# Optimization experiments

Measured on AMD Instinct MI355X. Metric: run time of the kernel, lower is better.

The kernel has to match this reference:

```python
import jax, jax.numpy as jnp
import numpy as np

ALPHA = 0.2  # LeakyReLU negative slope
NEG = -1e10  # mask value, matches -10000000000.0


def _gat_head(feat, adj, W, a1, a2):
    # feat: [N, Fin], W: [Fin, Fout], a1/a2: [Fout]
    h = feat @ W                              # [N, Fout]
    s = h @ a1                                # [N] attn_for_self
    t = h @ a2                                # [N] attn_for_neighs
    logits = jax.nn.leaky_relu(s[:, None] + t[None, :], ALPHA)  # [N, N]
    logits = logits + NEG * (1.0 - adj)       # additive adjacency mask
    attn = jax.nn.softmax(logits, axis=-1)    # [N, N]
    return attn @ h                           # [N, Fout]


def setup_inputs() -> dict:
    key = jax.random.key(0)
    ks = jax.random.split(key, 9)
    N, NFEAT, NHID, NCLASS, H = 6144, 128, 64, 16, 4
    glorot = jax.nn.initializers.glorot_uniform()
    adj = (jax.random.uniform(ks[0], (N, N)) < 0.005).astype(jnp.float32)
    feature = jax.random.normal(ks[1], (N, NFEAT), dtype=jnp.float32)
    in0 = NFEAT * H
    W0 = jnp.stack([glorot(ks[2 + i], (in0, NHID), jnp.float32) for i in range(H)])  # [H,in0,NHID]
    a1_0 = jax.random.normal(ks[6], (H, NHID), dtype=jnp.float32) * 0.1
    a2_0 = jax.random.normal(ks[7], (H, NHID), dtype=jnp.float32) * 0.1
    Wout = glorot(ks[8], (NHID * H, NCLASS), jnp.float32)
    a1_out = jax.random.normal(jax.random.fold_in(key, 100), (NCLASS,), dtype=jnp.float32) * 0.1
    a2_out = jax.random.normal(jax.random.fold_in(key, 101), (NCLASS,), dtype=jnp.float32) * 0.1
    return {"adj": adj, "feature": feature, "W0": W0, "a1_0": a1_0, "a2_0": a2_0,
            "Wout": Wout, "a1_out": a1_out, "a2_out": a2_out}


def reference(adj, feature, W0, a1_0, a2_0, Wout, a1_out, a2_out):
    H = W0.shape[0]
    N = feature.shape[0]
    x = jnp.tile(feature, (1, H))  # [N, nfeat*H]
    # hidden layer: H heads, concat=True -> elu then concat along features
    heads = jax.vmap(_gat_head, in_axes=(None, None, 0, 0, 0))(x, adj, W0, a1_0, a2_0)  # [H,N,NHID]
    heads = jax.nn.elu(heads)
    x = jnp.transpose(heads, (1, 0, 2)).reshape(N, -1)  # [N, H*NHID]
    # output layer: concat=False (no elu inside), then elu + softmax in GAT.call
    out = _gat_head(x, adj, Wout, a1_out, a2_out)  # [N, nclass]
    out = jax.nn.elu(out)
    return jax.nn.softmax(out, axis=-1)
```

## Files before the change

### kernel.cpp

```cpp
#include <hip/hip_runtime.h>
#include <cstdint>
#include <math.h>

#define N 6144
#define FIN 128
#define FH 64
#define NHEADS 4
#define NC 16
#define CAP 512
#define ALPHA 0.2f
#define NT 16

__device__ __forceinline__ float wave_sum(float v) {
    #pragma unroll
    for (int off = 32; off >= 1; off >>= 1) v += __shfl_xor(v, off);
    return v;
}
__device__ __forceinline__ float wave_max(float v) {
    #pragma unroll
    for (int off = 32; off >= 1; off >>= 1) v = fmaxf(v, __shfl_xor(v, off));
    return v;
}

__global__ void k_reduce_w(const float* __restrict__ W0, float* __restrict__ weff) {
    int idx = blockIdx.x * 256 + threadIdx.x;
    if (idx >= NHEADS * FIN * FH) return;
    int f = idx & 63, k = (idx >> 6) & 127, h = idx >> 13;
    const float* base = W0 + (size_t)h * 512 * 64;
    float s = 0.f;
    #pragma unroll
    for (int r = 0; r < 4; r++) s += base[(size_t)(r * 128 + k) * 64 + f];
    weff[idx] = s;
}

__global__ void k_hgemm(const float* __restrict__ feat, const float* __restrict__ weff,
                        const float* __restrict__ a1, const float* __restrict__ a2,
                        float* __restrict__ hfeat, float* __restrict__ sb,
                        float* __restrict__ tb) {
    __shared__ float fl[NT * FIN];
    int tid = threadIdx.x;
    int n0 = blockIdx.x * NT;
    for (int idx = tid; idx < NT * FIN; idx += 256) fl[idx] = feat[(size_t)n0 * FIN + idx];
    __syncthreads();
    int f = tid & 63, h = tid >> 6;
    const float* wcol = weff + (size_t)h * FIN * FH + f;
    float acc[NT];
    #pragma unroll
    for (int nn = 0; nn < NT; nn++) acc[nn] = 0.f;
    for (int k = 0; k < FIN; k++) {
        float w = wcol[(size_t)k * FH];
        #pragma unroll
        for (int nn = 0; nn < NT; nn++) acc[nn] = fmaf(fl[nn * FIN + k], w, acc[nn]);
    }
    float a1v = a1[h * FH + f], a2v = a2[h * FH + f];
    #pragma unroll
    for (int nn = 0; nn < NT; nn++) {
        hfeat[((size_t)h * N + (n0 + nn)) * FH + f] = acc[nn];
        float s = wave_sum(acc[nn] * a1v);
        float t = wave_sum(acc[nn] * a2v);
        if ((tid & 63) == 0) {
            sb[h * N + n0 + nn] = s;
            tb[h * N + n0 + nn] = t;
        }
    }
}

__global__ void k_row(const float* __restrict__ adj, const float* __restrict__ hfeat,
                      const float* __restrict__ sb, const float* __restrict__ tb,
                      const float* __restrict__ wout, const float* __restrict__ a1o,
                      const float* __restrict__ a2o,
                      int* __restrict__ cols, int* __restrict__ deg,
                      float* __restrict__ h2, float* __restrict__ s2,
                      float* __restrict__ t2) {
    int i = blockIdx.x;
    int tid = threadIdx.x;
    int lane = tid & 63, h = tid >> 6;
    __shared__ int lidx[CAP];
    __shared__ float xrow[NHEADS * FH];
    __shared__ int cnt;
    if (tid == 0) cnt = 0;
    __syncthreads();

    const float4* rowv = (const float4*)(adj + (size_t)i * N);
    float4 rv[6];
    #pragma unroll
    for (int it = 0; it < 6; it++) rv[it] = rowv[it * 256 + tid];
    unsigned long long lmask = (1ull << lane) - 1ull;
    #pragma unroll
    for (int it = 0; it < 6; it++) {
        int jb = (it * 256 + tid) * 4;
        bool p[4] = {rv[it].x != 0.f, rv[it].y != 0.f, rv[it].z != 0.f, rv[it].w != 0.f};
        #pragma unroll
        for (int c = 0; c < 4; c++) {
            unsigned long long mm = __ballot(p[c]);
            int tot = __popcll(mm);
            if (tot) {
                int prefix = __popcll(mm & lmask);
                int wb;
                if (lane == 0) wb = atomicAdd(&cnt, tot);
                wb = __shfl(wb, 0);
                int pos = wb + prefix;
                if (p[c] && pos < CAP) lidx[pos] = jb + c;
            }
        }
    }
    __syncthreads();
    int d = cnt;
    if (tid == 0) deg[i] = d;
    for (int t = tid; t < min(d, CAP); t += 256) cols[(size_t)i * CAP + t] = lidx[t];

    int mode = (d == 0) ? 1 : (d > CAP ? 2 : 0);
    int count = (mode == 0) ? d : N;
    const float* trow = tb + (size_t)h * N;
    const float* hrow = hfeat + (size_t)h * N * FH;
    float si = sb[h * N + i];
    int q = lane >> 4, fo = (lane & 15) * 4;
    float m = -INFINITY, l = 0.f;
    float4 acc = {0.f, 0.f, 0.f, 0.f};
    for (int base = 0; base < count; base += 64) {
        int idx = base + lane;
        int j = 0; float lr = -INFINITY;
        if (idx < count) {
            j = (mode == 0) ? lidx[idx] : idx;
            bool ok = (mode != 2) || (adj[(size_t)i * N + j] != 0.f);
            if (ok) {
                float z = si + trow[j];
                lr = (z >= 0.f) ? z : ALPHA * z;
            }
        }
        float mc = wave_max(lr);
        float mn = fmaxf(m, mc);
        if (mn == -INFINITY) continue;
        float scale = (m == -INFINITY) ? 0.f : expf(m - mn);
        float w = (lr == -INFINITY) ? 0.f : expf(lr - mn);
        l = l * scale + wave_sum(w);
        acc.x *= scale; acc.y *= scale; acc.z *= scale; acc.w *= scale;
        int cn = min(64, count - base);
        #pragma unroll 4
        for (int b = 0; b < cn; b += 4) {
            float wb = __shfl(w, b + q);
            int jn = __shfl(j, b + q);
            float4 hv = *(const float4*)(hrow + (size_t)jn * FH + fo);
            acc.x = fmaf(wb, hv.x, acc.x);
            acc.y = fmaf(wb, hv.y, acc.y);
            acc.z = fmaf(wb, hv.z, acc.z);
            acc.w = fmaf(wb, hv.w, acc.w);
        }
        m = mn;
    }
    #pragma unroll
    for (int off = 16; off <= 32; off <<= 1) {
        acc.x += __shfl_xor(acc.x, off);
        acc.y += __shfl_xor(acc.y, off);
        acc.z += __shfl_xor(acc.z, off);
        acc.w += __shfl_xor(acc.w, off);
    }
    if (lane < 16) {
        float linv = 1.f / l;
        float4 o;
        o.x = acc.x * linv; o.y = acc.y * linv; o.z = acc.z * linv; o.w = acc.w * linv;
        o.x = (o.x > 0.f) ? o.x : expm1f(o.x);
        o.y = (o.y > 0.f) ? o.y : expm1f(o.y);
        o.z = (o.z > 0.f) ? o.z : expm1f(o.z);
        o.w = (o.w > 0.f) ? o.w : expm1f(o.w);
        *(float4*)(xrow + h * FH + fo) = o;
    }
    __syncthreads();

    if (h == 0) {
        int f = lane & 15, part = lane >> 4;
        float dot = 0.f;
        #pragma unroll
        for (int k = 0; k < 64; k++)
            dot = fmaf(xrow[part * 64 + k], wout[(size_t)(part * 64 + k) * NC + f], dot);
        dot += __shfl_xor(dot, 16);
        dot += __shfl_xor(dot, 32);
        if (lane < NC) h2[(size_t)i * NC + lane] = dot;
        float sv = (lane < NC) ? dot * a1o[lane] : 0.f;
        float tv = (lane < NC) ? dot * a2o[lane] : 0.f;
        sv = wave_sum(sv); tv = wave_sum(tv);
        if (lane == 0) { s2[i] = sv; t2[i] = tv; }
    }
}

__global__ void k_attn_out(const float* __restrict__ h2, const float* __restrict__ s2,
                           const float* __restrict__ t2, const int* __restrict__ cols,
                           const int* __restrict__ deg, const float* __restrict__ adj,
                           float* __restrict__ out) {
    int w = threadIdx.x >> 6, lane = threadIdx.x & 63;
    int i = blockIdx.x * 4 + w;
    int d = deg[i];
    int mode = (d == 0) ? 1 : (d > CAP ? 2 : 0);
    int count = (mode == 0) ? d : N;
    const int* crow = cols + (size_t)i * CAP;
    float si = s2[i];
    int f = lane & 15, q = lane >> 4;
    float m = -INFINITY, l = 0.f, acc = 0.f;
    for (int base = 0; base < count; base += 64) {
        int idx = base + lane;
        int j = 0; float lr = -INFINITY;
        if (idx < count) {
            j = (mode == 0) ? crow[idx] : idx;
            bool ok = (mode != 2) || (adj[(size_t)i * N + j] != 0.f);
            if (ok) {
                float z = si + t2[j];
                lr = (z >= 0.f) ? z : ALPHA * z;
            }
        }
        float mc = wave_max(lr);
        float mn = fmaxf(m, mc);
        if (mn == -INFINITY) continue;
        float scale = (m == -INFINITY) ? 0.f : expf(m - mn);
        float wv = (lr == -INFINITY) ? 0.f : expf(lr - mn);
        l = l * scale + wave_sum(wv);
        acc *= scale;
        int cn = min(64, count - base);
        #pragma unroll 4
        for (int b = 0; b < cn; b += 4) {
            float wb = __shfl(wv, b + q);
            int jn = __shfl(j, b + q);
            acc = fmaf(wb, h2[(size_t)jn * NC + f], acc);
        }
        m = mn;
    }
    acc += __shfl_xor(acc, 16);
    acc += __shfl_xor(acc, 32);
    float o = acc / l;
    o = (o > 0.f) ? o : expm1f(o);
    float mv = (lane < NC) ? o : -INFINITY;
    float mx = wave_max(mv);
    float e = (lane < NC) ? expf(o - mx) : 0.f;
    float se = wave_sum(e);
    if (lane < NC) out[(size_t)i * NC + lane] = e / se;
}

extern "C" void kernel_launch(void* const* d_in, const int* in_sizes, int n_in,
                              void* d_out, int out_size, void* d_ws, size_t ws_size,
                              hipStream_t stream) {
    const float* adj  = (const float*)d_in[0];
    const float* feat = (const float*)d_in[1];
    const float* W0   = (const float*)d_in[2];
    const float* a1_0 = (const float*)d_in[3];
    const float* a2_0 = (const float*)d_in[4];
    const float* Wout = (const float*)d_in[5];
    const float* a1o  = (const float*)d_in[6];
    const float* a2o  = (const float*)d_in[7];
    float* out = (float*)d_out;

    float* weff  = (float*)d_ws;
    float* hfeat = weff + 32768;
    float* sb    = hfeat + 1572864;
    float* tb    = sb + 24576;
    float* h2    = tb + 24576;
    float* s2    = h2 + 98304;
    float* t2    = s2 + 6144;
    int*   cols  = (int*)(t2 + 6144);
    int*   deg   = cols + (size_t)N * CAP;

    k_reduce_w<<<128, 256, 0, stream>>>(W0, weff);
    k_hgemm<<<N / NT, 256, 0, stream>>>(feat, weff, a1_0, a2_0, hfeat, sb, tb);
    k_row<<<N, 256, 0, stream>>>(adj, hfeat, sb, tb, Wout, a1o, a2o,
                                 cols, deg, h2, s2, t2);
    k_attn_out<<<N / 4, 256, 0, stream>>>(h2, s2, t2, cols, deg, adj, out);
}
```

Before: 261.6 us.

## Fuse all four GAT stages into one cooperative persistent kernel with grid syncs

Replaces the four kernel launches with a single cooperative kernel of 512 blocks that runs weight reduction, the head GEMM, the per-row attention and the output attention as phases separated by grid.sync. Each block now handles 12 rows in sequence instead of one row per block, and the output phase loops over rows with one wave per row. This removes launch overhead and inter-kernel gaps. In exchange it brings in grid-wide barriers, fewer blocks in flight for latency hiding, and serial per-block row loops. The old four-kernel path is kept as a fallback if the cooperative launch fails.

```diff
diff --git a/kernel.cpp b/kernel.cpp
--- a/kernel.cpp
+++ b/kernel.cpp
@@ -1,6 +1,9 @@
 #include <hip/hip_runtime.h>
+#include <hip/hip_cooperative_groups.h>
 #include <cstdint>
 #include <math.h>
+
+namespace cg = cooperative_groups;
 
 #define N 6144
 #define FIN 128
@@ -9,6 +12,8 @@
 #define NC 16
 #define CAP 512
 #define ALPHA 0.2f
+#define NB 512
+#define RPB 12
 #define NT 16
 
 __device__ __forceinline__ float wave_sum(float v) {
@@ -20,6 +25,214 @@
     #pragma unroll
     for (int off = 32; off >= 1; off >>= 1) v = fmaxf(v, __shfl_xor(v, off));
     return v;
+}
+
+__global__ void __launch_bounds__(256, 4)
+k_fused(const float* __restrict__ adj, const float* __restrict__ feat,
+        const float* __restrict__ W0, const float* __restrict__ a1,
+        const float* __restrict__ a2, const float* __restrict__ wout,
+        const float* __restrict__ a1o, const float* __restrict__ a2o,
+        float* __restrict__ weff, float* __restrict__ hfeat,
+        float* __restrict__ sb, float* __restrict__ tb,
+        float* __restrict__ h2, float* __restrict__ s2, float* __restrict__ t2,
+        int* __restrict__ cols, int* __restrict__ deg, float* __restrict__ out)
+{
+    cg::grid_group grid = cg::this_grid();
+    int tid = threadIdx.x, lane = tid & 63, h = tid >> 6;
+    int b = blockIdx.x;
+
+    __shared__ float fl[RPB * FIN];
+    __shared__ int lidx[CAP];
+    __shared__ float xrow[NHEADS * FH];
+    __shared__ int cnt;
+
+    if (tid < 64) {
+        int idx = b * 64 + tid;
+        int f = idx & 63, k = (idx >> 6) & 127, hh = idx >> 13;
+        const float* base = W0 + (size_t)hh * 512 * 64;
+        float s = 0.f;
+        #pragma unroll
+        for (int r = 0; r < 4; r++) s += base[(size_t)(r * 128 + k) * 64 + f];
+        weff[idx] = s;
+    }
+    grid.sync();
+
+    {
+        int n0 = b * RPB;
+        for (int idx = tid; idx < RPB * FIN; idx += 256)
+            fl[idx] = feat[(size_t)n0 * FIN + idx];
+        __syncthreads();
+        const float* wcol = weff + (size_t)h * FIN * FH + lane;
+        float acc[RPB];
+        #pragma unroll
+        for (int nn = 0; nn < RPB; nn++) acc[nn] = 0.f;
+        for (int k = 0; k < FIN; k++) {
+            float w = wcol[(size_t)k * FH];
+            #pragma unroll
+            for (int nn = 0; nn < RPB; nn++) acc[nn] = fmaf(fl[nn * FIN + k], w, acc[nn]);
+        }
+        float a1v = a1[h * FH + lane], a2v = a2[h * FH + lane];
+        #pragma unroll
+        for (int nn = 0; nn < RPB; nn++) {
+            hfeat[((size_t)h * N + (n0 + nn)) * FH + lane] = acc[nn];
+            float s = wave_sum(acc[nn] * a1v);
+            float t = wave_sum(acc[nn] * a2v);
+            if (lane == 0) { sb[h * N + n0 + nn] = s; tb[h * N + n0 + nn] = t; }
+        }
+    }
+    grid.sync();
+
+    unsigned long long lmask = (1ull << lane) - 1ull;
+    for (int r = 0; r < RPB; r++) {
+        int i = b * RPB + r;
+        if (tid == 0) cnt = 0;
+        __syncthreads();
+        const float4* rowv = (const float4*)(adj + (size_t)i * N);
+        float4 rv[6];
+        #pragma unroll
+        for (int it = 0; it < 6; it++) rv[it] = rowv[it * 256 + tid];
+        #pragma unroll
+        for (int it = 0; it < 6; it++) {
+            int jb = (it * 256 + tid) * 4;
+            bool p[4] = {rv[it].x != 0.f, rv[it].y != 0.f, rv[it].z != 0.f, rv[it].w != 0.f};
+            #pragma unroll
+            for (int c = 0; c < 4; c++) {
+                unsigned long long mm = __ballot(p[c]);
+                int tot = __popcll(mm);
+                if (tot) {
+                    int prefix = __popcll(mm & lmask);
+                    int wb;
+                    if (lane == 0) wb = atomicAdd(&cnt, tot);
+                    wb = __shfl(wb, 0);
+                    int pos = wb + prefix;
+                    if (p[c] && pos < CAP) lidx[pos] = jb + c;
+                }
+            }
+        }
+        __syncthreads();
+        int d = cnt;
+        if (tid == 0) deg[i] = d;
+        for (int t = tid; t < min(d, CAP); t += 256) cols[(size_t)i * CAP + t] = lidx[t];
+
+        int mode = (d == 0) ? 1 : (d > CAP ? 2 : 0);
+        int count = (mode == 0) ? d : N;
+        const float* trow = tb + (size_t)h * N;
+        const float* hrow = hfeat + (size_t)h * N * FH;
+        float si = sb[h * N + i];
+        int q = lane >> 4, fo = (lane & 15) * 4;
+        float m = -INFINITY, l = 0.f;
+        float4 acc = {0.f, 0.f, 0.f, 0.f};
+        for (int base = 0; base < count; base += 64) {
+            int idx = base + lane;
+            int j = 0; float lr = -INFINITY;
+            if (idx < count) {
+                j = (mode == 0) ? lidx[idx] : idx;
+                bool ok = (mode != 2) || (adj[(size_t)i * N + j] != 0.f);
+                if (ok) {
+                    float z = si + trow[j];
+                    lr = (z >= 0.f) ? z : ALPHA * z;
+                }
+            }
+            float mc = wave_max(lr);
+            float mn = fmaxf(m, mc);
+            if (mn == -INFINITY) continue;
+            float scale = (m == -INFINITY) ? 0.f : expf(m - mn);
+            float w = (lr == -INFINITY) ? 0.f : expf(lr - mn);
+            l = l * scale + wave_sum(w);
+            acc.x *= scale; acc.y *= scale; acc.z *= scale; acc.w *= scale;
+            int cn = min(64, count - base);
+            #pragma unroll 4
+            for (int bb = 0; bb < cn; bb += 4) {
+                float wb = __shfl(w, bb + q);
+                int jn = __shfl(j, bb + q);
+                float4 hv = *(const float4*)(hrow + (size_t)jn * FH + fo);
+                acc.x = fmaf(wb, hv.x, acc.x);
+                acc.y = fmaf(wb, hv.y, acc.y);
+                acc.z = fmaf(wb, hv.z, acc.z);
+                acc.w = fmaf(wb, hv.w, acc.w);
+            }
+            m = mn;
+        }
+        #pragma unroll
+        for (int off = 16; off <= 32; off <<= 1) {
+            acc.x += __shfl_xor(acc.x, off);
+            acc.y += __shfl_xor(acc.y, off);
+            acc.z += __shfl_xor(acc.z, off);
+            acc.w += __shfl_xor(acc.w, off);
+        }
+        if (lane < 16) {
+            float linv = 1.f / l;
+            float4 o;
+            o.x = acc.x * linv; o.y = acc.y * linv; o.z = acc.z * linv; o.w = acc.w * linv;
+            o.x = (o.x > 0.f) ? o.x : expm1f(o.x);
+            o.y = (o.y > 0.f) ? o.y : expm1f(o.y);
+            o.z = (o.z > 0.f) ? o.z : expm1f(o.z);
+            o.w = (o.w > 0.f) ? o.w : expm1f(o.w);
+            *(float4*)(xrow + h * FH + fo) = o;
+        }
+        __syncthreads();
+        if (h == 0) {
+            int f = lane & 15, part = lane >> 4;
+            float dot = 0.f;
+            #pragma unroll
+            for (int k = 0; k < 64; k++)
+                dot = fmaf(xrow[part * 64 + k], wout[(size_t)(part * 64 + k) * NC + f], dot);
+            dot += __shfl_xor(dot, 16);
+            dot += __shfl_xor(dot, 32);
+            if (lane < NC) h2[(size_t)i * NC + lane] = dot;
+            float sv = (lane < NC) ? dot * a1o[lane] : 0.f;
+            float tv = (lane < NC) ? dot * a2o[lane] : 0.f;
+            sv = wave_sum(sv); tv = wave_sum(tv);
+            if (lane == 0) { s2[i] = sv; t2[i] = tv; }
+        }
+    }
+    grid.sync();
+
+    for (int i = b * NHEADS + h; i < N; i += NB * NHEADS) {
+        int d = deg[i];
+        int mode = (d == 0) ? 1 : (d > CAP ? 2 : 0);
+        int count = (mode == 0) ? d : N;
+        const int* crow = cols + (size_t)i * CAP;
+        float si = s2[i];
+        int f = lane & 15, q = lane >> 4;
+        float m = -INFINITY, l = 0.f, acc = 0.f;
+        for (int base = 0; base < count; base += 64) {
+            int idx = base + lane;
+            int j = 0; float lr = -INFINITY;
+            if (idx < count) {
+                j = (mode == 0) ? crow[idx] : idx;
+                bool ok = (mode != 2) || (adj[(size_t)i * N + j] != 0.f);
+                if (ok) {
+                    float z = si + t2[j];
+                    lr = (z >= 0.f) ? z : ALPHA * z;
+                }
+            }
+            float mc = wave_max(lr);
+            float mn = fmaxf(m, mc);
+            if (mn == -INFINITY) continue;
+            float scale = (m == -INFINITY) ? 0.f : expf(m - mn);
+            float wv = (lr == -INFINITY) ? 0.f : expf(lr - mn);
+            l = l * scale + wave_sum(wv);
+            acc *= scale;
+            int cn = min(64, count - base);
+            #pragma unroll 4
+            for (int bb = 0; bb < cn; bb += 4) {
+                float wb = __shfl(wv, bb + q);
+                int jn = __shfl(j, bb + q);
+                acc = fmaf(wb, h2[(size_t)jn * NC + f], acc);
+            }
+            m = mn;
+        }
+        acc += __shfl_xor(acc, 16);
+        acc += __shfl_xor(acc, 32);
+        float o = acc / l;
+        o = (o > 0.f) ? o : expm1f(o);
+        float mv = (lane < NC) ? o : -INFINITY;
+        float mx = wave_max(mv);
+        float e = (lane < NC) ? expf(o - mx) : 0.f;
+        float se = wave_sum(e);
+        if (lane < NC) out[(size_t)i * NC + lane] = e / se;
+    }
 }
 
 __global__ void k_reduce_w(const float* __restrict__ W0, float* __restrict__ weff) {
@@ -58,10 +271,7 @@
         hfeat[((size_t)h * N + (n0 + nn)) * FH + f] = acc[nn];
         float s = wave_sum(acc[nn] * a1v);
         float t = wave_sum(acc[nn] * a2v);
-        if ((tid & 63) == 0) {
-            sb[h * N + n0 + nn] = s;
-            tb[h * N + n0 + nn] = t;
-        }
+        if ((tid & 63) == 0) { sb[h * N + n0 + nn] = s; tb[h * N + n0 + nn] = t; }
     }
 }
 
@@ -80,7 +290,6 @@
     __shared__ int cnt;
     if (tid == 0) cnt = 0;
     __syncthreads();
-
     const float4* rowv = (const float4*)(adj + (size_t)i * N);
     float4 rv[6];
     #pragma unroll
@@ -137,9 +346,9 @@
         acc.x *= scale; acc.y *= scale; acc.z *= scale; acc.w *= scale;
         int cn = min(64, count - base);
         #pragma unroll 4
-        for (int b = 0; b < cn; b += 4) {
-            float wb = __shfl(w, b + q);
-            int jn = __shfl(j, b + q);
+        for (int bb = 0; bb < cn; bb += 4) {
+            float wb = __shfl(w, bb + q);
+            int jn = __shfl(j, bb + q);
             float4 hv = *(const float4*)(hrow + (size_t)jn * FH + fo);
             acc.x = fmaf(wb, hv.x, acc.x);
             acc.y = fmaf(wb, hv.y, acc.y);
@@ -166,7 +375,6 @@
         *(float4*)(xrow + h * FH + fo) = o;
     }
     __syncthreads();
-
     if (h == 0) {
         int f = lane & 15, part = lane >> 4;
         float dot = 0.f;
@@ -216,9 +424,9 @@
         acc *= scale;
         int cn = min(64, count - base);
         #pragma unroll 4
-        for (int b = 0; b < cn; b += 4) {
-            float wb = __shfl(wv, b + q);
-            int jn = __shfl(j, b + q);
+        for (int bb = 0; bb < cn; bb += 4) {
+            float wb = __shfl(wv, bb + q);
+            int jn = __shfl(j, bb + q);
             acc = fmaf(wb, h2[(size_t)jn * NC + f], acc);
         }
         m = mn;
@@ -245,7 +453,7 @@
     const float* Wout = (const float*)d_in[5];
     const float* a1o  = (const float*)d_in[6];
     const float* a2o  = (const float*)d_in[7];
-    float* out = (float*)d_out;
+    float* outp = (float*)d_out;
 
     float* weff  = (float*)d_ws;
     float* hfeat = weff + 32768;
@@ -257,9 +465,18 @@
     int*   cols  = (int*)(t2 + 6144);
     int*   deg   = cols + (size_t)N * CAP;
 
-    k_reduce_w<<<128, 256, 0, stream>>>(W0, weff);
-    k_hgemm<<<N / NT, 256, 0, stream>>>(feat, weff, a1_0, a2_0, hfeat, sb, tb);
-    k_row<<<N, 256, 0, stream>>>(adj, hfeat, sb, tb, Wout, a1o, a2o,
-                                 cols, deg, h2, s2, t2);
-    k_attn_out<<<N / 4, 256, 0, stream>>>(h2, s2, t2, cols, deg, adj, out);
-}
+    void* args[] = {(void*)&adj, (void*)&feat, (void*)&W0, (void*)&a1_0, (void*)&a2_0,
+                    (void*)&Wout, (void*)&a1o, (void*)&a2o,
+                    (void*)&weff, (void*)&hfeat, (void*)&sb, (void*)&tb,
+                    (void*)&h2, (void*)&s2, (void*)&t2,
+                    (void*)&cols, (void*)&deg, (void*)&outp};
+    hipError_t err = hipLaunchCooperativeKernel((const void*)k_fused, dim3(NB), dim3(256),
+                                                args, 0, stream);
+    if (err != hipSuccess) {
+        k_reduce_w<<<128, 256, 0, stream>>>(W0, weff);
+        k_hgemm<<<N / NT, 256, 0, stream>>>(feat, weff, a1_0, a2_0, hfeat, sb, tb);
+        k_row<<<N, 256, 0, stream>>>(adj, hfeat, sb, tb, Wout, a1o, a2o,
+                                     cols, deg, h2, s2, t2);
+        k_attn_out<<<N / 4, 256, 0, stream>>>(h2, s2, t2, cols, deg, adj, outp);
+    }
+}
```

New measurement: 593.6 us. +126.9%, slower.
